# Kernel optimization log

Measured on AMD Instinct MI355X. Metric: run time of the kernel, lower is better.

The kernel has to match this reference:

```python
import jax, jax.numpy as jnp
import numpy as np

B, T, E = 2048, 200, 64
H1, H2 = 64, 16
EPS = 1e-8


def dice(x, alpha):
    # Dice activation: standardize over (batch, seq) per feature, then
    # p = sigmoid(x_norm); out = p*x + (1-p)*alpha*x
    mean = jnp.mean(x, axis=(0, 1), keepdims=True)
    var = jnp.var(x, axis=(0, 1), keepdims=True)
    x_norm = (x - mean) * jax.lax.rsqrt(var + EPS)
    p = jax.nn.sigmoid(x_norm)
    return p * x + (1.0 - p) * alpha * x


def setup_inputs() -> dict:
    key = jax.random.key(0)
    ks = jax.random.split(key, 9)
    d_in = 4 * E
    return {
        "query_ad": jax.random.normal(ks[0], (B, 1, E), jnp.float32),
        "hist_behavior": jax.random.normal(ks[1], (B, T, E), jnp.float32),
        "hist_behavior_length": jax.random.randint(ks[2], (B,), 0, T, jnp.int64 if jax.config.jax_enable_x64 else jnp.int32),
        "W1": jax.random.normal(ks[3], (d_in, H1), jnp.float32) / np.sqrt(d_in),
        "b1": jnp.zeros((H1,), jnp.float32),
        "alpha1": jnp.zeros((H1,), jnp.float32),
        "W2": jax.random.normal(ks[4], (H1, H2), jnp.float32) / np.sqrt(H1),
        "b2": jnp.zeros((H2,), jnp.float32),
        "alpha2": jnp.zeros((H2,), jnp.float32),
    }


def reference(query_ad, hist_behavior, hist_behavior_length, W1, b1, alpha1, W2, b2, alpha2):
    Tlen = hist_behavior.shape[1]
    q = jnp.broadcast_to(query_ad, hist_behavior.shape)          # [B,T,E]
    att_in = jnp.concatenate(
        [q, hist_behavior, q - hist_behavior, q * hist_behavior], axis=-1
    )                                                            # [B,T,4E]
    h = dice(att_in @ W1 + b1, alpha1)                           # [B,T,H1]
    logits = dice(h @ W2 + b2, alpha2)                           # [B,T,H2]
    logits = jnp.swapaxes(logits, 1, 2)                          # [B,H2,T]
    mask = jnp.arange(Tlen)[None, :] < hist_behavior_length[:, None]  # [B,T]
    masked = jnp.where(mask[:, None, :], jnp.float32(1e-9), logits)
    score = jax.nn.softmax(masked, axis=-1)                      # [B,H2,T]
    out = jnp.einsum('bht,bte->bhe', score, hist_behavior)       # [B,H2,E]
    return out
```

## Files before the change

kernel.cpp:

```cpp
#include <hip/hip_runtime.h>
#include <math.h>


typedef float f4 __attribute__((ext_vector_type(4)));
typedef float f32x4 __attribute__((ext_vector_type(4)));
typedef short s8v __attribute__((ext_vector_type(8)));
typedef short s4v __attribute__((ext_vector_type(4)));
typedef unsigned short u16;

#define B_   2048
#define T_   200
#define BT_  409600
#define NB1  3200
#define NB2  1600

static __device__ __forceinline__ u16 f2bf(float f) {
  union { float f; unsigned u; } v; v.f = f;
  unsigned r = v.u + 0x7fffu + ((v.u >> 16) & 1u);
  return (u16)(r >> 16);
}
static __device__ __forceinline__ float bf2f(u16 s) {
  union { unsigned u; float f; } v; v.u = ((unsigned)s) << 16;
  return v.f;
}

__global__ __launch_bounds__(256) void k_qw(
    const float* __restrict__ q, const float* __restrict__ W1,
    const float* __restrict__ b1, float* __restrict__ qW,
    u16* __restrict__ wsWT) {
  __shared__ float Wac[64 * 65];
  __shared__ float ql[16 * 64];
  const int tid = threadIdx.x;
#pragma unroll
  for (int i = 0; i < 16; i++) {
    int idx = tid + 256 * i;
    int k = idx >> 6, j = idx & 63;
    Wac[k * 65 + j] = W1[k * 64 + j] + W1[(128 + k) * 64 + j];
  }
  const int b0 = blockIdx.x * 16;
#pragma unroll
  for (int i = 0; i < 4; i++) {
    int idx = tid + 256 * i;
    ql[idx] = q[(size_t)b0 * 64 + idx];
  }
  __syncthreads();
  const int wv = tid >> 6, lane = tid & 63;
#pragma unroll
  for (int ii = 0; ii < 4; ii++) {
    const int bl = wv * 4 + ii;
    float acc = b1[lane];
#pragma unroll 8
    for (int k = 0; k < 64; k++) acc += ql[bl * 64 + k] * Wac[k * 65 + lane];
    qW[(size_t)(b0 + bl) * 64 + lane] = acc;
  }
  if (blockIdx.x < 32) {
    int t = blockIdx.x * 256 + tid;
    int n = t >> 7, k = t & 127;
    float w = (k < 64) ? (W1[(64 + k) * 64 + n] - W1[(128 + k) * 64 + n])
                       : W1[(128 + k) * 64 + n];
    wsWT[t] = f2bf(w);
  }
}

__global__ __launch_bounds__(256, 3) void k_gemm1(
    const float* __restrict__ q, const float* __restrict__ hist,
    const u16* __restrict__ wsWT, const float* __restrict__ qW,
    u16* __restrict__ z1, float* __restrict__ part1) {
  __shared__ __align__(16) u16 As[128 * 136];
  __shared__ __align__(16) u16 Ws[64 * 136];
  const int tid = threadIdx.x;
  const int R0 = blockIdx.x * 128;

#pragma unroll
  for (int i = 0; i < 4; i++) {
    int piece = tid + 256 * i;
    int n = piece >> 4, k8 = piece & 15;
    *(s8v*)(Ws + n * 136 + 8 * k8) = *(const s8v*)(wsWT + n * 128 + 8 * k8);
  }
#pragma unroll
  for (int i = 0; i < 8; i++) {
    int piece = tid + 256 * i;
    int row = piece >> 4, c4 = piece & 15;
    int R = R0 + row;
    int b = (int)((unsigned)R / 200u);
    f4 h4 = *(const f4*)(hist + (size_t)R * 64 + 4 * c4);
    f4 q4 = *(const f4*)(q + (size_t)b * 64 + 4 * c4);
    f4 p4 = h4 * q4;
    s4v hv, pv;
#pragma unroll
    for (int j = 0; j < 4; j++) { hv[j] = (short)f2bf(h4[j]); pv[j] = (short)f2bf(p4[j]); }
    *(s4v*)(As + row * 136 + 4 * c4) = hv;
    *(s4v*)(As + row * 136 + 64 + 4 * c4) = pv;
  }
  __syncthreads();

  const int wv = tid >> 6, lane = tid & 63;
  const int lm16 = lane & 15, quad = lane >> 4;
  f32x4 acc[2][4];
#pragma unroll
  for (int mt = 0; mt < 2; mt++)
#pragma unroll
    for (int nt = 0; nt < 4; nt++) acc[mt][nt] = (f32x4)0.f;

#pragma unroll
  for (int c = 0; c < 4; c++) {
    const int ko = 32 * c + 8 * quad;
    s8v a0 = *(const s8v*)(As + (32 * wv + lm16) * 136 + ko);
    s8v a1 = *(const s8v*)(As + (32 * wv + 16 + lm16) * 136 + ko);
#pragma unroll
    for (int nt = 0; nt < 4; nt++) {
      s8v b8 = *(const s8v*)(Ws + (16 * nt + lm16) * 136 + ko);
      acc[0][nt] = __builtin_amdgcn_mfma_f32_16x16x32_bf16(a0, b8, acc[0][nt], 0, 0, 0);
      acc[1][nt] = __builtin_amdgcn_mfma_f32_16x16x32_bf16(a1, b8, acc[1][nt], 0, 0, 0);
    }
  }
  __syncthreads();

  u16* zs = As;
  float* red = (float*)Ws;
  const int g = wv * 4 + quad;
  float s[4] = {0.f, 0.f, 0.f, 0.f}, sq[4] = {0.f, 0.f, 0.f, 0.f};
#pragma unroll
  for (int mt = 0; mt < 2; mt++)
#pragma unroll
    for (int nt = 0; nt < 4; nt++)
#pragma unroll
      for (int r = 0; r < 4; r++) {
        int row = 32 * wv + 16 * mt + 4 * quad + r;
        int R = R0 + row;
        int b = (int)((unsigned)R / 200u);
        int col = 16 * nt + lm16;
        float v = acc[mt][nt][r] + qW[(size_t)b * 64 + col];
        s[nt] += v; sq[nt] += v * v;
        zs[row * 72 + col] = f2bf(v);
      }
#pragma unroll
  for (int nt = 0; nt < 4; nt++) {
    red[g * 64 + 16 * nt + lm16] = s[nt];
    red[1024 + g * 64 + 16 * nt + lm16] = sq[nt];
  }
  __syncthreads();
#pragma unroll
  for (int i = 0; i < 4; i++) {
    int piece = tid + 256 * i;
    int row = piece >> 3, seg = piece & 7;
    s8v v = *(const s8v*)(zs + row * 72 + 8 * seg);
    *(s8v*)(z1 + (size_t)(R0 + row) * 64 + 8 * seg) = v;
  }
  if (tid < 64) {
    float ss = 0.f, qq = 0.f;
#pragma unroll
    for (int gg = 0; gg < 16; gg++) { ss += red[gg * 64 + tid]; qq += red[1024 + gg * 64 + tid]; }
    part1[(size_t)blockIdx.x * 128 + tid] = ss;
    part1[(size_t)blockIdx.x * 128 + 64 + tid] = qq;
  }
}

__global__ __launch_bounds__(256) void k_finalize(
    const float* __restrict__ part, float* __restrict__ statout,
    int nj, int stride, int nb, float invN) {
  const int j = blockIdx.x, tid = threadIdx.x;
  float s = 0.f, qq = 0.f;
  for (int i = tid; i < nb; i += 256) {
    s += part[(size_t)i * stride + j];
    qq += part[(size_t)i * stride + nj + j];
  }
#pragma unroll
  for (int off = 32; off > 0; off >>= 1) {
    s += __shfl_down(s, off);
    qq += __shfl_down(qq, off);
  }
  __shared__ float rs[4], rq[4];
  if ((tid & 63) == 0) { rs[tid >> 6] = s; rq[tid >> 6] = qq; }
  __syncthreads();
  if (tid == 0) {
    s = rs[0] + rs[1] + rs[2] + rs[3];
    qq = rq[0] + rq[1] + rq[2] + rq[3];
    float mean = s * invN;
    float var = qq * invN - mean * mean;
    statout[j] = mean;
    statout[nj + j] = rsqrtf(var + 1e-8f);
  }
}

__global__ __launch_bounds__(256) void k_gemm2(
    const u16* __restrict__ z1, const float* __restrict__ W2g,
    const float* __restrict__ b2, const float* __restrict__ alpha1,
    const float* __restrict__ stat1, u16* __restrict__ z2,
    float* __restrict__ part2) {
  __shared__ float W2l[64 * 16];
  __shared__ float cf[208];
  __shared__ float red[256 * 33];
  const int tid = threadIdx.x;
  if (tid < 64) {
    cf[tid] = stat1[tid];
    cf[64 + tid] = stat1[64 + tid];
    cf[128 + tid] = alpha1[tid];
  }
  if (tid < 16) cf[192 + tid] = b2[tid];
#pragma unroll
  for (int i = 0; i < 4; i++) { int idx = tid + 256 * i; W2l[idx] = W2g[idx]; }
  __syncthreads();
  const size_t row = (size_t)blockIdx.x * 256 + tid;
  const u16* zr = z1 + row * 64;
  float acc[16];
#pragma unroll
  for (int j = 0; j < 16; j++) acc[j] = cf[192 + j];
  for (int k0 = 0; k0 < 64; k0 += 8) {
    s8v x8 = *(const s8v*)(zr + k0);
#pragma unroll
    for (int dk = 0; dk < 8; dk++) {
      int k = k0 + dk;
      float x = bf2f((u16)x8[dk]);
      float xn = (x - cf[k]) * cf[64 + k];
      float p = 1.f / (1.f + __expf(-xn));
      float h = x * (p + (1.f - p) * cf[128 + k]);
#pragma unroll
      for (int jc = 0; jc < 4; jc++) {
        f4 w = *(const f4*)(W2l + k * 16 + 4 * jc);
#pragma unroll
        for (int jj = 0; jj < 4; jj++) acc[4 * jc + jj] += h * w[jj];
      }
    }
  }
  s8v o0, o1;
#pragma unroll
  for (int jj = 0; jj < 8; jj++) { o0[jj] = (short)f2bf(acc[jj]); o1[jj] = (short)f2bf(acc[8 + jj]); }
  *(s8v*)(z2 + row * 16) = o0;
  *(s8v*)(z2 + row * 16 + 8) = o1;
#pragma unroll
  for (int j = 0; j < 16; j++) {
    red[tid * 33 + j] = acc[j];
    red[tid * 33 + 16 + j] = acc[j] * acc[j];
  }
  __syncthreads();
  const int f = tid >> 3, sub = tid & 7;
  float s = 0.f;
  for (int g = sub; g < 256; g += 8) s += red[g * 33 + f];
  s += __shfl_down(s, 4, 8);
  s += __shfl_down(s, 2, 8);
  s += __shfl_down(s, 1, 8);
  if (sub == 0) part2[(size_t)blockIdx.x * 32 + f] = s;
}

__global__ __launch_bounds__(256, 3) void k_attn(
    const float* __restrict__ hist, const u16* __restrict__ z2,
    const int* __restrict__ lens, const float* __restrict__ alpha2,
    const float* __restrict__ stat2, float* __restrict__ out) {
  __shared__ float lm[200 * 17];
  __shared__ __align__(16) u16 scb[16 * 232];
  __shared__ __align__(16) u16 hT[64 * 232];
  __shared__ float cf2[48];
  const int tid = threadIdx.x;
  const int b = blockIdx.x;
  const int L = lens[b];
  if (tid < 16) {
    cf2[tid] = stat2[tid];
    cf2[16 + tid] = stat2[16 + tid];
    cf2[32 + tid] = alpha2[tid];
  }
  __syncthreads();
  {
    s8v zz = {0, 0, 0, 0, 0, 0, 0, 0};
    for (int p = tid; p < 320; p += 256) {
      if (p < 64) { int r = p >> 2, c = p & 3; *(s8v*)(scb + r * 232 + 200 + 8 * c) = zz; }
      else { int pp = p - 64; int r = pp >> 2, c = pp & 3; *(s8v*)(hT + r * 232 + 200 + 8 * c) = zz; }
    }
  }
  const float* hb = hist + (size_t)b * 200 * 64;
#pragma unroll
  for (int i = 0; i < 13; i++) {
    int p = tid + 256 * i;
    if (p < 3200) {
      int t = p >> 4, eq = p & 15;
      f4 h4 = *(const f4*)(hb + t * 64 + 4 * eq);
#pragma unroll
      for (int jj = 0; jj < 4; jj++) hT[(4 * eq + jj) * 232 + t] = f2bf(h4[jj]);
    }
  }
  if (tid < 200) {
    const u16* zr = z2 + ((size_t)b * 200 + tid) * 16;
    s8v x0 = *(const s8v*)zr, x1 = *(const s8v*)(zr + 8);
#pragma unroll
    for (int j = 0; j < 16; j++) {
      float x = bf2f((u16)(j < 8 ? x0[j] : x1[j - 8]));
      float xn = (x - cf2[j]) * cf2[16 + j];
      float p = 1.f / (1.f + __expf(-xn));
      float lg = x * (p + (1.f - p) * cf2[32 + j]);
      lm[tid * 17 + j] = (tid < L) ? 1e-9f : lg;
    }
  }
  __syncthreads();
  {
    const int h = tid >> 4, s = tid & 15;
    float v[13];
    float m = -1e30f;
#pragma unroll
    for (int i = 0; i < 13; i++) {
      int t = s + 16 * i;
      float x = (t < 200) ? lm[t * 17 + h] : -1e30f;
      v[i] = x;
      m = fmaxf(m, x);
    }
#pragma unroll
    for (int mk = 8; mk > 0; mk >>= 1) m = fmaxf(m, __shfl_xor(m, mk, 16));
    float sum = 0.f;
#pragma unroll
    for (int i = 0; i < 13; i++) {
      int t = s + 16 * i;
      if (t < 200) { float e = __expf(v[i] - m); v[i] = e; sum += e; }
    }
#pragma unroll
    for (int mk = 8; mk > 0; mk >>= 1) sum += __shfl_xor(sum, mk, 16);
    const float inv = 1.f / sum;
#pragma unroll
    for (int i = 0; i < 13; i++) {
      int t = s + 16 * i;
      if (t < 200) scb[h * 232 + t] = f2bf(v[i] * inv);
    }
  }
  __syncthreads();
  {
    const int wv = tid >> 6, lane = tid & 63;
    const int lm16 = lane & 15, quad = lane >> 4;
    f32x4 acc = {0.f, 0.f, 0.f, 0.f};
#pragma unroll
    for (int c = 0; c < 7; c++) {
      const int ko = 32 * c + 8 * quad;
      s8v a = *(const s8v*)(scb + lm16 * 232 + ko);
      s8v bb = *(const s8v*)(hT + (16 * wv + lm16) * 232 + ko);
      acc = __builtin_amdgcn_mfma_f32_16x16x32_bf16(a, bb, acc, 0, 0, 0);
    }
#pragma unroll
    for (int r = 0; r < 4; r++) {
      int h = 4 * quad + r;
      out[(size_t)b * 1024 + h * 64 + 16 * wv + lm16] = acc[r];
    }
  }
}

extern "C" void kernel_launch(void* const* d_in, const int* in_sizes, int n_in,
                              void* d_out, int out_size, void* d_ws, size_t ws_size,
                              hipStream_t stream) {
  const float* q    = (const float*)d_in[0];
  const float* hist = (const float*)d_in[1];
  const int*   len  = (const int*)d_in[2];
  const float* W1   = (const float*)d_in[3];
  const float* b1   = (const float*)d_in[4];
  const float* al1  = (const float*)d_in[5];
  const float* W2   = (const float*)d_in[6];
  const float* b2   = (const float*)d_in[7];
  const float* al2  = (const float*)d_in[8];
  float* out = (float*)d_out;

  char* ws = (char*)d_ws;
  u16*   z1    = (u16*)ws;
  u16*   z2    = (u16*)(ws + 52428800);
  float* qW    = (float*)(ws + 52428800 + 13107200);
  u16*   wsWT  = (u16*)((char*)qW + 524288);
  float* part1 = (float*)((char*)wsWT + 16384);
  float* part2 = part1 + (size_t)NB1 * 128;
  float* stat1 = part2 + (size_t)NB2 * 32;
  float* stat2 = stat1 + 128;
  (void)ws_size; (void)in_sizes; (void)n_in; (void)out_size;

  k_qw<<<dim3(128), dim3(256), 0, stream>>>(q, W1, b1, qW, wsWT);
  k_gemm1<<<dim3(NB1), dim3(256), 0, stream>>>(q, hist, wsWT, qW, z1, part1);
  k_finalize<<<dim3(64), dim3(256), 0, stream>>>(part1, stat1, 64, 128, NB1, 1.f / (float)BT_);
  k_gemm2<<<dim3(NB2), dim3(256), 0, stream>>>(z1, W2, b2, al1, stat1, z2, part2);
  k_finalize<<<dim3(16), dim3(256), 0, stream>>>(part2, stat2, 16, 32, NB2, 1.f / (float)BT_);
  k_attn<<<dim3(B_), dim3(256), 0, stream>>>(hist, z2, len, al2, stat2, out);
}
```

Measured before the change: 255.6 us.

## Trim LDS use and batch global loads across gemm1, gemm2 and attention kernels

In k_gemm1 the bf16 weight tile is no longer staged in LDS; MFMA B operands are read straight from global/L2. The two possible batch rows of q and qW are cached in a small shared array, so there is no per-element divide or global gather, and the hist loads are issued into registers up front. Occupancy hints are raised. k_gemm2 prefetches its whole z1 row before the barrier and halves the reduction scratch by reducing sum and sum-of-squares in two passes. k_attn drops one barrier and transposes hist into LDS with 4x4 blocks, writing vectorized 4-element stores. The risks are extra barriers in k_gemm2 and B-operand fetches from global in k_gemm1 that now depend on cache hits.

```diff
diff --git a/kernel.cpp b/kernel.cpp
--- a/kernel.cpp
+++ b/kernel.cpp
@@ -62,29 +62,39 @@
   }
 }
 
-__global__ __launch_bounds__(256, 3) void k_gemm1(
+__global__ __launch_bounds__(256, 4) void k_gemm1(
     const float* __restrict__ q, const float* __restrict__ hist,
     const u16* __restrict__ wsWT, const float* __restrict__ qW,
     u16* __restrict__ z1, float* __restrict__ part1) {
   __shared__ __align__(16) u16 As[128 * 136];
-  __shared__ __align__(16) u16 Ws[64 * 136];
+  __shared__ __align__(16) float qs[256];
   const int tid = threadIdx.x;
   const int R0 = blockIdx.x * 128;
-
-#pragma unroll
-  for (int i = 0; i < 4; i++) {
-    int piece = tid + 256 * i;
-    int n = piece >> 4, k8 = piece & 15;
-    *(s8v*)(Ws + n * 136 + 8 * k8) = *(const s8v*)(wsWT + n * 128 + 8 * k8);
-  }
+  const int bb0 = (int)((unsigned)R0 / 200u);
+  const int off0 = R0 - bb0 * 200;
+  const int bb1 = (bb0 + 1 < B_) ? bb0 + 1 : B_ - 1;
+
+  if (tid < 64) {
+    int sel = tid >> 4, o4 = (tid & 15) * 4;
+    const float* src = (sel < 2 ? q : qW) + (size_t)((sel & 1) ? bb1 : bb0) * 64 + o4;
+    *(f4*)(qs + sel * 64 + o4) = *(const f4*)src;
+  }
+  f4 hreg[8];
 #pragma unroll
   for (int i = 0; i < 8; i++) {
     int piece = tid + 256 * i;
     int row = piece >> 4, c4 = piece & 15;
-    int R = R0 + row;
-    int b = (int)((unsigned)R / 200u);
-    f4 h4 = *(const f4*)(hist + (size_t)R * 64 + 4 * c4);
-    f4 q4 = *(const f4*)(q + (size_t)b * 64 + 4 * c4);
+    hreg[i] = *(const f4*)(hist + (size_t)(R0 + row) * 64 + 4 * c4);
+  }
+  __syncthreads();
+
+#pragma unroll
+  for (int i = 0; i < 8; i++) {
+    int piece = tid + 256 * i;
+    int row = piece >> 4, c4 = piece & 15;
+    int bsel = (off0 + row) >= 200;
+    f4 h4 = hreg[i];
+    f4 q4 = *(const f4*)(qs + bsel * 64 + 4 * c4);
     f4 p4 = h4 * q4;
     s4v hv, pv;
 #pragma unroll
@@ -109,7 +119,7 @@
     s8v a1 = *(const s8v*)(As + (32 * wv + 16 + lm16) * 136 + ko);
 #pragma unroll
     for (int nt = 0; nt < 4; nt++) {
-      s8v b8 = *(const s8v*)(Ws + (16 * nt + lm16) * 136 + ko);
+      s8v b8 = *(const s8v*)(wsWT + (16 * nt + lm16) * 128 + ko);
       acc[0][nt] = __builtin_amdgcn_mfma_f32_16x16x32_bf16(a0, b8, acc[0][nt], 0, 0, 0);
       acc[1][nt] = __builtin_amdgcn_mfma_f32_16x16x32_bf16(a1, b8, acc[1][nt], 0, 0, 0);
     }
@@ -117,7 +127,7 @@
   __syncthreads();
 
   u16* zs = As;
-  float* red = (float*)Ws;
+  float* red = (float*)(As + 128 * 72);
   const int g = wv * 4 + quad;
   float s[4] = {0.f, 0.f, 0.f, 0.f}, sq[4] = {0.f, 0.f, 0.f, 0.f};
 #pragma unroll
@@ -127,10 +137,9 @@
 #pragma unroll
       for (int r = 0; r < 4; r++) {
         int row = 32 * wv + 16 * mt + 4 * quad + r;
-        int R = R0 + row;
-        int b = (int)((unsigned)R / 200u);
+        int bsel = (off0 + row) >= 200;
         int col = 16 * nt + lm16;
-        float v = acc[mt][nt][r] + qW[(size_t)b * 64 + col];
+        float v = acc[mt][nt][r] + qs[128 + bsel * 64 + col];
         s[nt] += v; sq[nt] += v * v;
         zs[row * 72 + col] = f2bf(v);
       }
@@ -183,14 +192,14 @@
   }
 }
 
-__global__ __launch_bounds__(256) void k_gemm2(
+__global__ __launch_bounds__(256, 6) void k_gemm2(
     const u16* __restrict__ z1, const float* __restrict__ W2g,
     const float* __restrict__ b2, const float* __restrict__ alpha1,
     const float* __restrict__ stat1, u16* __restrict__ z2,
     float* __restrict__ part2) {
   __shared__ float W2l[64 * 16];
   __shared__ float cf[208];
-  __shared__ float red[256 * 33];
+  __shared__ float red[256 * 17];
   const int tid = threadIdx.x;
   if (tid < 64) {
     cf[tid] = stat1[tid];
@@ -200,18 +209,21 @@
   if (tid < 16) cf[192 + tid] = b2[tid];
 #pragma unroll
   for (int i = 0; i < 4; i++) { int idx = tid + 256 * i; W2l[idx] = W2g[idx]; }
-  __syncthreads();
   const size_t row = (size_t)blockIdx.x * 256 + tid;
   const u16* zr = z1 + row * 64;
+  s8v xv[8];
+#pragma unroll
+  for (int i = 0; i < 8; i++) xv[i] = *(const s8v*)(zr + 8 * i);
+  __syncthreads();
   float acc[16];
 #pragma unroll
   for (int j = 0; j < 16; j++) acc[j] = cf[192 + j];
-  for (int k0 = 0; k0 < 64; k0 += 8) {
-    s8v x8 = *(const s8v*)(zr + k0);
+#pragma unroll
+  for (int i = 0; i < 8; i++) {
 #pragma unroll
     for (int dk = 0; dk < 8; dk++) {
-      int k = k0 + dk;
-      float x = bf2f((u16)x8[dk]);
+      int k = 8 * i + dk;
+      float x = bf2f((u16)xv[i][dk]);
       float xn = (x - cf[k]) * cf[64 + k];
       float p = 1.f / (1.f + __expf(-xn));
       float h = x * (p + (1.f - p) * cf[128 + k]);
@@ -229,18 +241,34 @@
   *(s8v*)(z2 + row * 16) = o0;
   *(s8v*)(z2 + row * 16 + 8) = o1;
 #pragma unroll
-  for (int j = 0; j < 16; j++) {
-    red[tid * 33 + j] = acc[j];
-    red[tid * 33 + 16 + j] = acc[j] * acc[j];
-  }
-  __syncthreads();
-  const int f = tid >> 3, sub = tid & 7;
-  float s = 0.f;
-  for (int g = sub; g < 256; g += 8) s += red[g * 33 + f];
-  s += __shfl_down(s, 4, 8);
-  s += __shfl_down(s, 2, 8);
-  s += __shfl_down(s, 1, 8);
-  if (sub == 0) part2[(size_t)blockIdx.x * 32 + f] = s;
+  for (int j = 0; j < 16; j++) red[tid * 17 + j] = acc[j];
+  __syncthreads();
+  {
+    const int f = tid >> 4, sub = tid & 15;
+    float s = 0.f;
+#pragma unroll
+    for (int i = 0; i < 16; i++) s += red[(sub + 16 * i) * 17 + f];
+    s += __shfl_down(s, 8, 16);
+    s += __shfl_down(s, 4, 16);
+    s += __shfl_down(s, 2, 16);
+    s += __shfl_down(s, 1, 16);
+    if (sub == 0) part2[(size_t)blockIdx.x * 32 + f] = s;
+  }
+  __syncthreads();
+#pragma unroll
+  for (int j = 0; j < 16; j++) red[tid * 17 + j] = acc[j] * acc[j];
+  __syncthreads();
+  {
+    const int f = tid >> 4, sub = tid & 15;
+    float s = 0.f;
+#pragma unroll
+    for (int i = 0; i < 16; i++) s += red[(sub + 16 * i) * 17 + f];
+    s += __shfl_down(s, 8, 16);
+    s += __shfl_down(s, 4, 16);
+    s += __shfl_down(s, 2, 16);
+    s += __shfl_down(s, 1, 16);
+    if (sub == 0) part2[(size_t)blockIdx.x * 32 + 16 + f] = s;
+  }
 }
 
 __global__ __launch_bounds__(256, 3) void k_attn(
@@ -259,7 +287,6 @@
     cf2[16 + tid] = stat2[16 + tid];
     cf2[32 + tid] = alpha2[tid];
   }
-  __syncthreads();
   {
     s8v zz = {0, 0, 0, 0, 0, 0, 0, 0};
     for (int p = tid; p < 320; p += 256) {
@@ -269,13 +296,22 @@
   }
   const float* hb = hist + (size_t)b * 200 * 64;
 #pragma unroll
-  for (int i = 0; i < 13; i++) {
-    int p = tid + 256 * i;
-    if (p < 3200) {
-      int t = p >> 4, eq = p & 15;
-      f4 h4 = *(const f4*)(hb + t * 64 + 4 * eq);
-#pragma unroll
-      for (int jj = 0; jj < 4; jj++) hT[(4 * eq + jj) * 232 + t] = f2bf(h4[jj]);
+  for (int l = 0; l < 4; l++) {
+    int p = tid + 256 * l;
+    if (p < 800) {
+      int tg = p >> 4, eg = p & 15;
+      int t0 = 4 * tg, e0 = 4 * eg;
+      f4 r0 = *(const f4*)(hb + (size_t)(t0 + 0) * 64 + e0);
+      f4 r1 = *(const f4*)(hb + (size_t)(t0 + 1) * 64 + e0);
+      f4 r2 = *(const f4*)(hb + (size_t)(t0 + 2) * 64 + e0);
+      f4 r3 = *(const f4*)(hb + (size_t)(t0 + 3) * 64 + e0);
+#pragma unroll
+      for (int j = 0; j < 4; j++) {
+        s4v sv;
+        sv[0] = (short)f2bf(r0[j]); sv[1] = (short)f2bf(r1[j]);
+        sv[2] = (short)f2bf(r2[j]); sv[3] = (short)f2bf(r3[j]);
+        *(s4v*)(hT + (e0 + j) * 232 + t0) = sv;
+      }
     }
   }
   if (tid < 200) {
```

Result: slower. 274.6 us (+7.5%).
